# Kernel optimization log

Measured on AMD Instinct MI355X. Metric: run time of the kernel, lower is better.

The kernel has to match this reference:

```python
import jax, jax.numpy as jnp
import numpy as np

N_NODES = 100000
N_EDGES = 3200000
LEAKY_SLOPE = 0.01  # torch F.leaky_relu default


def _conv(x, W, b, src, dst):
    # DGL-style custom GCN conv: sum-aggregate neighbor features, then linear.
    msgs = x[src]                                            # [E, d_in]
    agg = jax.ops.segment_sum(msgs, dst, num_segments=N_NODES)  # [N, d_in]
    return agg @ W + b                                       # [N, d_out]


def setup_inputs() -> dict:
    key = jax.random.key(0)
    ks = jax.random.split(key, 8)
    features = jax.random.normal(ks[0], (N_NODES, 4), dtype=jnp.float32)
    src = jax.random.randint(ks[1], (N_EDGES,), 0, N_NODES, dtype=jnp.int32)
    dst = jax.random.randint(ks[2], (N_EDGES,), 0, N_NODES, dtype=jnp.int32)
    # Kaiming-ish init scale
    W1 = jax.random.normal(ks[3], (4, 64), dtype=jnp.float32) * (1.0 / np.sqrt(4))
    b1 = jnp.zeros((64,), dtype=jnp.float32)
    W2 = jax.random.normal(ks[4], (64, 64), dtype=jnp.float32) * (1.0 / np.sqrt(64))
    b2 = jnp.zeros((64,), dtype=jnp.float32)
    W5 = jax.random.normal(ks[5], (64, 3), dtype=jnp.float32) * (1.0 / np.sqrt(64))
    b5 = jnp.zeros((3,), dtype=jnp.float32)
    return {"features": features, "src": src, "dst": dst,
            "W1": W1, "b1": b1, "W2": W2, "b2": b2, "W5": W5, "b5": b5}


def reference(features, src, dst, W1, b1, W2, b2, W5, b5):
    lrelu = lambda v: jax.nn.leaky_relu(v, negative_slope=LEAKY_SLOPE)
    x = lrelu(_conv(features, W1, b1, src, dst))
    # layer2 weights are shared across 7 applications (as in the torch module)
    for _ in range(7):
        x = lrelu(_conv(x, W2, b2, src, dst))
    x = _conv(x, W5, b5, src, dst)
    return x
```

## Files before the change

kernel.cpp:

```cpp
#include <hip/hip_runtime.h>

#define N_NODES 100000
#define N_EDGES 3200000
#define SLOPE 0.01f

#define NBUCK 391
#define NBLK_B 256
#define EPB (N_EDGES / NBLK_B)
#define NGH (NBUCK * NBLK_B)
#define CAP_C 10240

typedef __attribute__((ext_vector_type(8))) short short8;
typedef __attribute__((ext_vector_type(4))) float f32x4;

static inline size_t align_up(size_t x, size_t a){ return (x + a - 1) / a * a; }

__device__ inline unsigned short f2bf(float f){
  unsigned u = __float_as_uint(f);
  u += 0x7fffu + ((u >> 16) & 1u);
  return (unsigned short)(u >> 16);
}
__device__ inline float bf2f(unsigned short s){
  return __uint_as_float(((unsigned)s) << 16);
}
__device__ inline void add2(float& a0, float& a1, unsigned u){
  a0 += __uint_as_float(u << 16);
  a1 += __uint_as_float(u & 0xffff0000u);
}


__global__ void gbhist_k(const int* __restrict__ dst, int* __restrict__ ghist){
  __shared__ int h[NBUCK];
  int tid = threadIdx.x, blk = blockIdx.x;
  for (int i = tid; i < NBUCK; i += 256) h[i] = 0;
  __syncthreads();
  int e0 = blk * EPB;
  for (int e = e0 + tid; e < e0 + EPB; e += 256) atomicAdd(&h[dst[e] >> 8], 1);
  __syncthreads();
  for (int i = tid; i < NBUCK; i += 256) ghist[i * NBLK_B + blk] = h[i];
}

__global__ void scan1_k(const int* __restrict__ in, int* __restrict__ out,
                        int* __restrict__ bsums, int n){
  __shared__ int lds[256];
  int tid = threadIdx.x;
  int base = blockIdx.x * 1024 + tid * 4;
  int v0 = (base + 0 < n) ? in[base + 0] : 0;
  int v1 = (base + 1 < n) ? in[base + 1] : 0;
  int v2 = (base + 2 < n) ? in[base + 2] : 0;
  int v3 = (base + 3 < n) ? in[base + 3] : 0;
  int tsum = v0 + v1 + v2 + v3;
  lds[tid] = tsum;
  for (int off = 1; off < 256; off <<= 1){
    __syncthreads();
    int x = (tid >= off) ? lds[tid - off] : 0;
    __syncthreads();
    lds[tid] += x;
  }
  __syncthreads();
  int excl = lds[tid] - tsum;
  if (base + 0 < n) out[base + 0] = excl;
  if (base + 1 < n) out[base + 1] = excl + v0;
  if (base + 2 < n) out[base + 2] = excl + v0 + v1;
  if (base + 3 < n) out[base + 3] = excl + v0 + v1 + v2;
  if (tid == 255) bsums[blockIdx.x] = lds[255];
}

__global__ void scan2_k(int* bsums, int nb){
  int lane = threadIdx.x;
  int base = 0;
  for (int off = 0; off < nb; off += 64){
    int idx = off + lane;
    int v = (idx < nb) ? bsums[idx] : 0;
    int sc = v;
    for (int m = 1; m < 64; m <<= 1){
      int t = __shfl_up(sc, m);
      if (lane >= m) sc += t;
    }
    int total = __shfl(sc, 63);
    if (idx < nb) bsums[idx] = sc - v + base;
    base += total;
  }
}

__global__ void scan3_k(int* __restrict__ out, const int* __restrict__ bsums,
                        int n, int set_end){
  int i = blockIdx.x * 256 + threadIdx.x;
  if (i < n) out[i] += bsums[i >> 10];
  else if (i == n && set_end) out[n] = N_EDGES;
}

__global__ void passB_k(const int* __restrict__ src, const int* __restrict__ dst,
                        const int* __restrict__ goff, int* __restrict__ pk){
  __shared__ int h[NBUCK];
  __shared__ int buf[EPB];
  int tid = threadIdx.x, blk = blockIdx.x;
  for (int i = tid; i < NBUCK; i += 256) h[i] = 0;
  __syncthreads();
  int e0 = blk * EPB;
  for (int e = e0 + tid; e < e0 + EPB; e += 256) atomicAdd(&h[dst[e] >> 8], 1);
  __syncthreads();
  if (tid < 64){
    int base = 0;
    for (int off = 0; off < NBUCK; off += 64){
      int idx = off + tid;
      int v = (idx < NBUCK) ? h[idx] : 0;
      int sc = v;
      for (int m = 1; m < 64; m <<= 1){
        int t = __shfl_up(sc, m);
        if (tid >= m) sc += t;
      }
      int total = __shfl(sc, 63);
      if (idx < NBUCK) h[idx] = sc - v + base;
      base += total;
    }
  }
  __syncthreads();
  for (int e = e0 + tid; e < e0 + EPB; e += 256){
    int d = dst[e];
    int p = atomicAdd(&h[d >> 8], 1);
    buf[p] = (src[e] << 8) | (d & 255);
  }
  __syncthreads();
  int wv = tid >> 6, ln = tid & 63;
  for (int b = wv; b < NBUCK; b += 4){
    int s0 = (b == 0) ? 0 : h[b - 1];
    int L  = h[b] - s0;
    int g0 = goff[b * NBLK_B + blk];
    for (int j = ln; j < L; j += 64) pk[g0 + j] = buf[s0 + j];
  }
}

__global__ void histnode_k(const int* __restrict__ pk, const int* __restrict__ goff,
                           int* __restrict__ counts){
  __shared__ int cnt[256];
  int b = blockIdx.x, tid = threadIdx.x;
  if (tid < 256) cnt[tid] = 0;
  __syncthreads();
  int s = goff[b * NBLK_B];
  int e = (b == NBUCK - 1) ? N_EDGES : goff[(b + 1) * NBLK_B];
  for (int i = s + tid; i < e; i += 512) atomicAdd(&cnt[pk[i] & 255], 1);
  __syncthreads();
  int node = b * 256 + tid;
  if (tid < 256 && node < N_NODES) counts[node] = cnt[tid];
}

__global__ void passC_k(const int* __restrict__ pk, const int* __restrict__ goff,
                        int* __restrict__ ssrc){
  __shared__ int cur[256];
  __shared__ int buf[CAP_C];
  int b = blockIdx.x, tid = threadIdx.x;
  if (tid < 256) cur[tid] = 0;
  __syncthreads();
  int s = goff[b * NBLK_B];
  int e = (b == NBUCK - 1) ? N_EDGES : goff[(b + 1) * NBLK_B];
  int cnt = e - s;
  for (int i = s + tid; i < e; i += 512) atomicAdd(&cur[pk[i] & 255], 1);
  __syncthreads();
  if (tid < 64){
    int base = 0;
    for (int off = 0; off < 256; off += 64){
      int idx = off + tid;
      int v = cur[idx];
      int sc = v;
      for (int m = 1; m < 64; m <<= 1){
        int t = __shfl_up(sc, m);
        if (tid >= m) sc += t;
      }
      int total = __shfl(sc, 63);
      cur[idx] = sc - v + base;
      base += total;
    }
  }
  __syncthreads();
  for (int i = s + tid; i < e; i += 512){
    int v = pk[i];
    int p = atomicAdd(&cur[v & 255], 1);
    if (p < CAP_C) buf[p] = v >> 8;
    else ssrc[s + p] = v >> 8;
  }
  __syncthreads();
  int lim = (cnt < CAP_C) ? cnt : CAP_C;
  for (int i = tid; i < lim; i += 512) ssrc[s + i] = buf[i];
}

__global__ void conv1_k(const float* __restrict__ feat, const int* __restrict__ row_ptr,
                        const int* __restrict__ ssrc, const float* __restrict__ W1,
                        const float* __restrict__ b1, unsigned short* __restrict__ out){
  int gt = blockIdx.x * 256 + threadIdx.x;
  int node = gt >> 6;
  int lane = threadIdx.x & 63;
  int s = row_ptr[node], t = row_ptr[node + 1];
  float a0 = 0.f, a1 = 0.f, a2 = 0.f, a3 = 0.f;
  for (int i = s + lane; i < t; i += 64){
    int nb = ssrc[i];
    const float4 v = *(const float4*)(feat + (size_t)nb * 4);
    a0 += v.x; a1 += v.y; a2 += v.z; a3 += v.w;
  }
  for (int m = 1; m < 64; m <<= 1){
    a0 += __shfl_xor(a0, m);
    a1 += __shfl_xor(a1, m);
    a2 += __shfl_xor(a2, m);
    a3 += __shfl_xor(a3, m);
  }
  float o = b1[lane] + a0 * W1[lane] + a1 * W1[64 + lane] + a2 * W1[128 + lane] + a3 * W1[192 + lane];
  o = (o > 0.f) ? o : SLOPE * o;
  out[node * 64 + lane] = f2bf(o);
}

__global__ void mm64_k(const unsigned short* __restrict__ x, const float* __restrict__ W,
                       unsigned short* __restrict__ z){
  int lane = threadIdx.x & 63;
  int wid = (blockIdx.x * blockDim.x + threadIdx.x) >> 6;
  int nwaves = (gridDim.x * blockDim.x) >> 6;
  int r = lane & 15, g = lane >> 4;
  short8 Af[4][2];
  #pragma unroll
  for (int mb = 0; mb < 4; ++mb)
    #pragma unroll
    for (int kt = 0; kt < 2; ++kt){
      short8 f;
      #pragma unroll
      for (int j = 0; j < 8; ++j){
        int k = kt * 32 + g * 8 + j;
        f[j] = (short)f2bf(W[k * 64 + mb * 16 + r]);
      }
      Af[mb][kt] = f;
    }
  const int NT = N_NODES / 16;
  for (int t = wid; t < NT; t += nwaves){
    int base = t * 16;
    const short8 B0 = *(const short8*)(x + (size_t)(base + r) * 64 + g * 8);
    const short8 B1 = *(const short8*)(x + (size_t)(base + r) * 64 + 32 + g * 8);
    #pragma unroll
    for (int mb = 0; mb < 4; ++mb){
      f32x4 c = {0.f, 0.f, 0.f, 0.f};
      c = __builtin_amdgcn_mfma_f32_16x16x32_bf16(Af[mb][0], B0, c, 0, 0, 0);
      c = __builtin_amdgcn_mfma_f32_16x16x32_bf16(Af[mb][1], B1, c, 0, 0, 0);
      ushort4 pk4;
      pk4.x = f2bf(c[0]); pk4.y = f2bf(c[1]); pk4.z = f2bf(c[2]); pk4.w = f2bf(c[3]);
      *(ushort4*)(z + (size_t)(base + r) * 64 + mb * 16 + g * 4) = pk4;
    }
  }
}

__global__ void agg64_k(const unsigned short* __restrict__ z, const int* __restrict__ row_ptr,
                        const int* __restrict__ ssrc, const float* __restrict__ b,
                        unsigned short* __restrict__ out){
  int gt = blockIdx.x * 256 + threadIdx.x;
  int node = gt >> 6;
  int lane = threadIdx.x & 63;
  int s = row_ptr[node], cnt = row_ptr[node + 1] - s;
  int nb_l = ssrc[s + lane];
  int q = lane >> 3, o = lane & 7;
  float a0=0.f,a1=0.f,a2=0.f,a3=0.f,a4=0.f,a5=0.f,a6=0.f,a7=0.f;
  uint4 v0, v1, v2, v3, v4, v5;
  int cm1 = (cnt > 0) ? cnt - 1 : 0;
  {
    int j0 = min( 0 + q, cm1), j1 = min( 8 + q, cm1), j2 = min(16 + q, cm1);
    int j3 = min(24 + q, cm1), j4 = min(32 + q, cm1), j5 = min(40 + q, cm1);
    int n0 = __shfl(nb_l, j0), n1 = __shfl(nb_l, j1), n2 = __shfl(nb_l, j2);
    int n3 = __shfl(nb_l, j3), n4 = __shfl(nb_l, j4), n5 = __shfl(nb_l, j5);
    const size_t oo = (size_t)(o << 3);
    v0 = *(const uint4*)(z + (size_t)n0 * 64 + oo);
    v1 = *(const uint4*)(z + (size_t)n1 * 64 + oo);
    v2 = *(const uint4*)(z + (size_t)n2 * 64 + oo);
    v3 = *(const uint4*)(z + (size_t)n3 * 64 + oo);
    v4 = *(const uint4*)(z + (size_t)n4 * 64 + oo);
    v5 = *(const uint4*)(z + (size_t)n5 * 64 + oo);
  }
  if ( 0 + q < cnt){ add2(a0,a1,v0.x); add2(a2,a3,v0.y); add2(a4,a5,v0.z); add2(a6,a7,v0.w); }
  if ( 8 + q < cnt){ add2(a0,a1,v1.x); add2(a2,a3,v1.y); add2(a4,a5,v1.z); add2(a6,a7,v1.w); }
  if (16 + q < cnt){ add2(a0,a1,v2.x); add2(a2,a3,v2.y); add2(a4,a5,v2.z); add2(a6,a7,v2.w); }
  if (24 + q < cnt){ add2(a0,a1,v3.x); add2(a2,a3,v3.y); add2(a4,a5,v3.z); add2(a6,a7,v3.w); }
  if (32 + q < cnt){ add2(a0,a1,v4.x); add2(a2,a3,v4.y); add2(a4,a5,v4.z); add2(a6,a7,v4.w); }
  if (40 + q < cnt){ add2(a0,a1,v5.x); add2(a2,a3,v5.y); add2(a4,a5,v5.z); add2(a6,a7,v5.w); }
  for (int i = 48 + q; i < cnt; i += 8){
    int nb = ssrc[s + i];
    uint4 vv = *(const uint4*)(z + (size_t)nb * 64 + (size_t)(o << 3));
    add2(a0,a1,vv.x); add2(a2,a3,vv.y); add2(a4,a5,vv.z); add2(a6,a7,vv.w);
  }
  for (int m = 8; m < 64; m <<= 1){
    a0 += __shfl_xor(a0, m); a1 += __shfl_xor(a1, m);
    a2 += __shfl_xor(a2, m); a3 += __shfl_xor(a3, m);
    a4 += __shfl_xor(a4, m); a5 += __shfl_xor(a5, m);
    a6 += __shfl_xor(a6, m); a7 += __shfl_xor(a7, m);
  }
  if (lane < 8){
    const float4 bA = *(const float4*)(b + lane * 8);
    const float4 bB = *(const float4*)(b + lane * 8 + 4);
    float y0 = a0 + bA.x, y1 = a1 + bA.y, y2 = a2 + bA.z, y3 = a3 + bA.w;
    float y4 = a4 + bB.x, y5 = a5 + bB.y, y6 = a6 + bB.z, y7 = a7 + bB.w;
    y0 = (y0 > 0.f) ? y0 : SLOPE * y0;  y1 = (y1 > 0.f) ? y1 : SLOPE * y1;
    y2 = (y2 > 0.f) ? y2 : SLOPE * y2;  y3 = (y3 > 0.f) ? y3 : SLOPE * y3;
    y4 = (y4 > 0.f) ? y4 : SLOPE * y4;  y5 = (y5 > 0.f) ? y5 : SLOPE * y5;
    y6 = (y6 > 0.f) ? y6 : SLOPE * y6;  y7 = (y7 > 0.f) ? y7 : SLOPE * y7;
    uint4 pkd;
    pkd.x = (unsigned)f2bf(y0) | ((unsigned)f2bf(y1) << 16);
    pkd.y = (unsigned)f2bf(y2) | ((unsigned)f2bf(y3) << 16);
    pkd.z = (unsigned)f2bf(y4) | ((unsigned)f2bf(y5) << 16);
    pkd.w = (unsigned)f2bf(y6) | ((unsigned)f2bf(y7) << 16);
    *(uint4*)(out + (size_t)node * 64 + lane * 8) = pkd;
  }
}

__global__ void premult_k(const unsigned short* __restrict__ x, const float* __restrict__ W5,
                          float* __restrict__ y4){
  int gt = blockIdx.x * 256 + threadIdx.x;
  int node = gt >> 6;
  int lane = threadIdx.x & 63;
  float xv = bf2f(x[node * 64 + lane]);
  float p0 = xv * W5[lane * 3 + 0];
  float p1 = xv * W5[lane * 3 + 1];
  float p2 = xv * W5[lane * 3 + 2];
  for (int m = 1; m < 64; m <<= 1){
    p0 += __shfl_xor(p0, m);
    p1 += __shfl_xor(p1, m);
    p2 += __shfl_xor(p2, m);
  }
  if (lane == 0){
    float4 v; v.x = p0; v.y = p1; v.z = p2; v.w = 0.f;
    *(float4*)(y4 + (size_t)node * 4) = v;
  }
}

__global__ void agg3_k(const float* __restrict__ y4, const int* __restrict__ row_ptr,
                       const int* __restrict__ ssrc, const float* __restrict__ b5,
                       float* __restrict__ out){
  int gt = blockIdx.x * 256 + threadIdx.x;
  int node = gt >> 6;
  int lane = threadIdx.x & 63;
  int s = row_ptr[node], t = row_ptr[node + 1];
  int c = lane & 3;
  float acc = 0.f;
  for (int i = s + (lane >> 2); i < t; i += 16) acc += y4[(size_t)ssrc[i] * 4 + c];
  for (int m = 4; m < 64; m <<= 1) acc += __shfl_xor(acc, m);
  if (lane < 3) out[node * 3 + lane] = acc + b5[lane];
}


extern "C" void kernel_launch(void* const* d_in, const int* in_sizes, int n_in,
                              void* d_out, int out_size, void* d_ws, size_t ws_size,
                              hipStream_t stream){
  const float* feat = (const float*)d_in[0];
  const int*   src  = (const int*)d_in[1];
  const int*   dst  = (const int*)d_in[2];
  const float* W1   = (const float*)d_in[3];
  const float* b1   = (const float*)d_in[4];
  const float* W2   = (const float*)d_in[5];
  const float* b2   = (const float*)d_in[6];
  const float* W5   = (const float*)d_in[7];
  const float* b5   = (const float*)d_in[8];
  float* out = (float*)d_out;

  char* p = (char*)d_ws;
  auto carve = [&](size_t bytes) -> char* {
    char* r = p; p += align_up(bytes, 512); return r;
  };
  int*   counts  = (int*)carve((size_t)N_NODES * 4);
  int*   row_ptr = (int*)carve((size_t)(N_NODES + 1) * 4);
  int*   bsums   = (int*)carve(512 * 4);
  int*   ghist   = (int*)carve((size_t)NGH * 4);
  int*   goff    = (int*)carve((size_t)NGH * 4);
  int*   ssrc    = (int*)carve(((size_t)N_EDGES + 64) * 4);
  unsigned short* bufA = (unsigned short*)carve((size_t)N_NODES * 64 * 2);
  unsigned short* bufB = (unsigned short*)carve((size_t)N_NODES * 64 * 2);
  float* y4      = (float*)carve((size_t)N_NODES * 4 * 4);
  int*   pk      = (int*)carve((size_t)N_EDGES * 4);
  unsigned short* zbuf = (unsigned short*)pk;

  gbhist_k<<<NBLK_B, 256, 0, stream>>>(dst, ghist);
  {
    int nb = (NGH + 1023) / 1024;
    scan1_k<<<nb, 256, 0, stream>>>(ghist, goff, bsums, NGH);
    scan2_k<<<1, 64, 0, stream>>>(bsums, nb);
    scan3_k<<<(NGH + 256) / 256, 256, 0, stream>>>(goff, bsums, NGH, 0);
  }
  passB_k<<<NBLK_B, 256, 0, stream>>>(src, dst, goff, pk);
  histnode_k<<<NBUCK, 512, 0, stream>>>(pk, goff, counts);
  {
    int nb = (N_NODES + 1023) / 1024;
    scan1_k<<<nb, 256, 0, stream>>>(counts, row_ptr, bsums, N_NODES);
    scan2_k<<<1, 64, 0, stream>>>(bsums, nb);
    scan3_k<<<(N_NODES + 256) / 256, 256, 0, stream>>>(row_ptr, bsums, N_NODES, 1);
  }
  passC_k<<<NBUCK, 512, 0, stream>>>(pk, goff, ssrc);
  hipMemsetAsync(ssrc + N_EDGES, 0, 64 * 4, stream);

  conv1_k<<<(N_NODES * 64) / 256, 256, 0, stream>>>(feat, row_ptr, ssrc, W1, b1, bufA);

  unsigned short* xin = bufA;
  unsigned short* xout = bufB;
  for (int l = 0; l < 7; ++l){
    mm64_k<<<512, 256, 0, stream>>>(xin, W2, zbuf);
    agg64_k<<<(N_NODES * 64) / 256, 256, 0, stream>>>(zbuf, row_ptr, ssrc, b2, xout);
    unsigned short* tmp = xin; xin = xout; xout = tmp;
  }

  premult_k<<<(N_NODES * 64) / 256, 256, 0, stream>>>(xin, W5, y4);
  agg3_k<<<(N_NODES * 64) / 256, 256, 0, stream>>>(y4, row_ptr, ssrc, b5, out);
}
```

Baseline: 633.2 us.

## Fuse CSR build passes: derive row_ptr in passC, reuse bucket histogram

Removes the separate per-node histogram kernel and the three-kernel scan for row_ptr. passC now writes row_ptr directly from its local prefix sums plus the bucket offset. passB reuses the global histogram from gbhist instead of recounting destinations. The histogram and partition kernels move to 1024-thread blocks. agg64 now issues neighbor loads only when the degree makes them needed and skips per-lane bounds checks for full groups of eight, which adds branch divergence in exchange for fewer wasted gathers.

```diff
diff --git a/kernel.cpp b/kernel.cpp
--- a/kernel.cpp
+++ b/kernel.cpp
@@ -32,12 +32,12 @@
 __global__ void gbhist_k(const int* __restrict__ dst, int* __restrict__ ghist){
   __shared__ int h[NBUCK];
   int tid = threadIdx.x, blk = blockIdx.x;
-  for (int i = tid; i < NBUCK; i += 256) h[i] = 0;
+  for (int i = tid; i < NBUCK; i += 1024) h[i] = 0;
   __syncthreads();
   int e0 = blk * EPB;
-  for (int e = e0 + tid; e < e0 + EPB; e += 256) atomicAdd(&h[dst[e] >> 8], 1);
-  __syncthreads();
-  for (int i = tid; i < NBUCK; i += 256) ghist[i * NBLK_B + blk] = h[i];
+  for (int e = e0 + tid; e < e0 + EPB; e += 1024) atomicAdd(&h[dst[e] >> 8], 1);
+  __syncthreads();
+  for (int i = tid; i < NBUCK; i += 1024) ghist[i * NBLK_B + blk] = h[i];
 }
 
 __global__ void scan1_k(const int* __restrict__ in, int* __restrict__ out,
@@ -83,22 +83,18 @@
   }
 }
 
-__global__ void scan3_k(int* __restrict__ out, const int* __restrict__ bsums,
-                        int n, int set_end){
+__global__ void scan3_k(int* __restrict__ out, const int* __restrict__ bsums, int n){
   int i = blockIdx.x * 256 + threadIdx.x;
   if (i < n) out[i] += bsums[i >> 10];
-  else if (i == n && set_end) out[n] = N_EDGES;
 }
 
 __global__ void passB_k(const int* __restrict__ src, const int* __restrict__ dst,
-                        const int* __restrict__ goff, int* __restrict__ pk){
+                        const int* __restrict__ ghist, const int* __restrict__ goff,
+                        int* __restrict__ pk){
   __shared__ int h[NBUCK];
   __shared__ int buf[EPB];
   int tid = threadIdx.x, blk = blockIdx.x;
-  for (int i = tid; i < NBUCK; i += 256) h[i] = 0;
-  __syncthreads();
-  int e0 = blk * EPB;
-  for (int e = e0 + tid; e < e0 + EPB; e += 256) atomicAdd(&h[dst[e] >> 8], 1);
+  for (int i = tid; i < NBUCK; i += 1024) h[i] = ghist[i * NBLK_B + blk];
   __syncthreads();
   if (tid < 64){
     int base = 0;
@@ -116,14 +112,15 @@
     }
   }
   __syncthreads();
-  for (int e = e0 + tid; e < e0 + EPB; e += 256){
+  int e0 = blk * EPB;
+  for (int e = e0 + tid; e < e0 + EPB; e += 1024){
     int d = dst[e];
     int p = atomicAdd(&h[d >> 8], 1);
     buf[p] = (src[e] << 8) | (d & 255);
   }
   __syncthreads();
   int wv = tid >> 6, ln = tid & 63;
-  for (int b = wv; b < NBUCK; b += 4){
+  for (int b = wv; b < NBUCK; b += 16){
     int s0 = (b == 0) ? 0 : h[b - 1];
     int L  = h[b] - s0;
     int g0 = goff[b * NBLK_B + blk];
@@ -131,22 +128,8 @@
   }
 }
 
-__global__ void histnode_k(const int* __restrict__ pk, const int* __restrict__ goff,
-                           int* __restrict__ counts){
-  __shared__ int cnt[256];
-  int b = blockIdx.x, tid = threadIdx.x;
-  if (tid < 256) cnt[tid] = 0;
-  __syncthreads();
-  int s = goff[b * NBLK_B];
-  int e = (b == NBUCK - 1) ? N_EDGES : goff[(b + 1) * NBLK_B];
-  for (int i = s + tid; i < e; i += 512) atomicAdd(&cnt[pk[i] & 255], 1);
-  __syncthreads();
-  int node = b * 256 + tid;
-  if (tid < 256 && node < N_NODES) counts[node] = cnt[tid];
-}
-
 __global__ void passC_k(const int* __restrict__ pk, const int* __restrict__ goff,
-                        int* __restrict__ ssrc){
+                        int* __restrict__ ssrc, int* __restrict__ row_ptr){
   __shared__ int cur[256];
   __shared__ int buf[CAP_C];
   int b = blockIdx.x, tid = threadIdx.x;
@@ -172,6 +155,10 @@
       base += total;
     }
   }
+  __syncthreads();
+  int node = b * 256 + tid;
+  if (tid < 256 && node < N_NODES) row_ptr[node] = s + cur[tid];
+  if (b == NBUCK - 1 && tid == 0) row_ptr[N_NODES] = N_EDGES;
   __syncthreads();
   for (int i = s + tid; i < e; i += 512){
     int v = pk[i];
@@ -253,31 +240,27 @@
   int s = row_ptr[node], cnt = row_ptr[node + 1] - s;
   int nb_l = ssrc[s + lane];
   int q = lane >> 3, o = lane & 7;
+  const size_t oo = (size_t)(o << 3);
   float a0=0.f,a1=0.f,a2=0.f,a3=0.f,a4=0.f,a5=0.f,a6=0.f,a7=0.f;
+  int cm1 = (cnt > 0) ? cnt - 1 : 0;
   uint4 v0, v1, v2, v3, v4, v5;
-  int cm1 = (cnt > 0) ? cnt - 1 : 0;
-  {
-    int j0 = min( 0 + q, cm1), j1 = min( 8 + q, cm1), j2 = min(16 + q, cm1);
-    int j3 = min(24 + q, cm1), j4 = min(32 + q, cm1), j5 = min(40 + q, cm1);
-    int n0 = __shfl(nb_l, j0), n1 = __shfl(nb_l, j1), n2 = __shfl(nb_l, j2);
-    int n3 = __shfl(nb_l, j3), n4 = __shfl(nb_l, j4), n5 = __shfl(nb_l, j5);
-    const size_t oo = (size_t)(o << 3);
-    v0 = *(const uint4*)(z + (size_t)n0 * 64 + oo);
-    v1 = *(const uint4*)(z + (size_t)n1 * 64 + oo);
-    v2 = *(const uint4*)(z + (size_t)n2 * 64 + oo);
-    v3 = *(const uint4*)(z + (size_t)n3 * 64 + oo);
-    v4 = *(const uint4*)(z + (size_t)n4 * 64 + oo);
-    v5 = *(const uint4*)(z + (size_t)n5 * 64 + oo);
-  }
-  if ( 0 + q < cnt){ add2(a0,a1,v0.x); add2(a2,a3,v0.y); add2(a4,a5,v0.z); add2(a6,a7,v0.w); }
-  if ( 8 + q < cnt){ add2(a0,a1,v1.x); add2(a2,a3,v1.y); add2(a4,a5,v1.z); add2(a6,a7,v1.w); }
-  if (16 + q < cnt){ add2(a0,a1,v2.x); add2(a2,a3,v2.y); add2(a4,a5,v2.z); add2(a6,a7,v2.w); }
-  if (24 + q < cnt){ add2(a0,a1,v3.x); add2(a2,a3,v3.y); add2(a4,a5,v3.z); add2(a6,a7,v3.w); }
-  if (32 + q < cnt){ add2(a0,a1,v4.x); add2(a2,a3,v4.y); add2(a4,a5,v4.z); add2(a6,a7,v4.w); }
-  if (40 + q < cnt){ add2(a0,a1,v5.x); add2(a2,a3,v5.y); add2(a4,a5,v5.z); add2(a6,a7,v5.w); }
+  if (cnt >  0){ int n = __shfl(nb_l, min( 0 + q, cm1)); v0 = *(const uint4*)(z + (size_t)n * 64 + oo); }
+  if (cnt >  8){ int n = __shfl(nb_l, min( 8 + q, cm1)); v1 = *(const uint4*)(z + (size_t)n * 64 + oo); }
+  if (cnt > 16){ int n = __shfl(nb_l, min(16 + q, cm1)); v2 = *(const uint4*)(z + (size_t)n * 64 + oo); }
+  if (cnt > 24){ int n = __shfl(nb_l, min(24 + q, cm1)); v3 = *(const uint4*)(z + (size_t)n * 64 + oo); }
+  if (cnt > 32){ int n = __shfl(nb_l, min(32 + q, cm1)); v4 = *(const uint4*)(z + (size_t)n * 64 + oo); }
+  if (cnt > 40){ int n = __shfl(nb_l, min(40 + q, cm1)); v5 = *(const uint4*)(z + (size_t)n * 64 + oo); }
+  #define ACC(V) { add2(a0,a1,V.x); add2(a2,a3,V.y); add2(a4,a5,V.z); add2(a6,a7,V.w); }
+  if (cnt >  0){ if (cnt >=  8) ACC(v0) else { if ( 0 + q < cnt) ACC(v0) } }
+  if (cnt >  8){ if (cnt >= 16) ACC(v1) else { if ( 8 + q < cnt) ACC(v1) } }
+  if (cnt > 16){ if (cnt >= 24) ACC(v2) else { if (16 + q < cnt) ACC(v2) } }
+  if (cnt > 24){ if (cnt >= 32) ACC(v3) else { if (24 + q < cnt) ACC(v3) } }
+  if (cnt > 32){ if (cnt >= 40) ACC(v4) else { if (32 + q < cnt) ACC(v4) } }
+  if (cnt > 40){ if (cnt >= 48) ACC(v5) else { if (40 + q < cnt) ACC(v5) } }
+  #undef ACC
   for (int i = 48 + q; i < cnt; i += 8){
     int nb = ssrc[s + i];
-    uint4 vv = *(const uint4*)(z + (size_t)nb * 64 + (size_t)(o << 3));
+    uint4 vv = *(const uint4*)(z + (size_t)nb * 64 + oo);
     add2(a0,a1,vv.x); add2(a2,a3,vv.y); add2(a4,a5,vv.z); add2(a6,a7,vv.w);
   }
   for (int m = 8; m < 64; m <<= 1){
@@ -357,7 +340,6 @@
   auto carve = [&](size_t bytes) -> char* {
     char* r = p; p += align_up(bytes, 512); return r;
   };
-  int*   counts  = (int*)carve((size_t)N_NODES * 4);
   int*   row_ptr = (int*)carve((size_t)(N_NODES + 1) * 4);
   int*   bsums   = (int*)carve(512 * 4);
   int*   ghist   = (int*)carve((size_t)NGH * 4);
@@ -369,22 +351,15 @@
   int*   pk      = (int*)carve((size_t)N_EDGES * 4);
   unsigned short* zbuf = (unsigned short*)pk;
 
-  gbhist_k<<<NBLK_B, 256, 0, stream>>>(dst, ghist);
+  gbhist_k<<<NBLK_B, 1024, 0, stream>>>(dst, ghist);
   {
     int nb = (NGH + 1023) / 1024;
     scan1_k<<<nb, 256, 0, stream>>>(ghist, goff, bsums, NGH);
     scan2_k<<<1, 64, 0, stream>>>(bsums, nb);
-    scan3_k<<<(NGH + 256) / 256, 256, 0, stream>>>(goff, bsums, NGH, 0);
-  }
-  passB_k<<<NBLK_B, 256, 0, stream>>>(src, dst, goff, pk);
-  histnode_k<<<NBUCK, 512, 0, stream>>>(pk, goff, counts);
-  {
-    int nb = (N_NODES + 1023) / 1024;
-    scan1_k<<<nb, 256, 0, stream>>>(counts, row_ptr, bsums, N_NODES);
-    scan2_k<<<1, 64, 0, stream>>>(bsums, nb);
-    scan3_k<<<(N_NODES + 256) / 256, 256, 0, stream>>>(row_ptr, bsums, N_NODES, 1);
-  }
-  passC_k<<<NBUCK, 512, 0, stream>>>(pk, goff, ssrc);
+    scan3_k<<<(NGH + 255) / 256, 256, 0, stream>>>(goff, bsums, NGH);
+  }
+  passB_k<<<NBLK_B, 1024, 0, stream>>>(src, dst, ghist, goff, pk);
+  passC_k<<<NBUCK, 512, 0, stream>>>(pk, goff, ssrc, row_ptr);
   hipMemsetAsync(ssrc + N_EDGES, 0, 64 * 4, stream);
 
   conv1_k<<<(N_NODES * 64) / 256, 256, 0, stream>>>(feat, row_ptr, ssrc, W1, b1, bufA);
```

Result: faster. 606.5 us (-4.2%).
